# Kernel tuning notes

Measured on AMD Instinct MI355X. Metric: run time of the kernel, lower is better.

The kernel has to match this reference:

```python
import jax, jax.numpy as jnp
import numpy as np

N_HEADS = 16
HEAD_DIM = 64
DIM = 1024
B, L = 2, 2048


def setup_inputs() -> dict:
    key = jax.random.key(0)
    ks = jax.random.split(key, 6)
    s = 1.0 / np.sqrt(DIM)
    return {
        "X": jax.random.normal(ks[0], (B, L, DIM), dtype=jnp.float32),
        "attention_mask": jax.random.randint(ks[1], (B, L, L), 0, 2, dtype=jnp.int32),
        "Wq": jax.random.normal(ks[2], (DIM, DIM), dtype=jnp.float32) * s,
        "Wk": jax.random.normal(ks[3], (DIM, DIM), dtype=jnp.float32) * s,
        "Wv": jax.random.normal(ks[4], (DIM, DIM), dtype=jnp.float32) * s,
        "Wo": jax.random.normal(ks[5], (DIM, DIM), dtype=jnp.float32) * s,
    }


def reference(X, attention_mask, Wq, Wk, Wv, Wo):
    # Linear weights follow torch convention: (out_features, in_features)
    b, l, _ = X.shape
    Q = (X @ Wq.T).reshape(b, l, N_HEADS, HEAD_DIM).transpose(0, 2, 1, 3)  # [B,H,L,D]
    K = (X @ Wk.T).reshape(b, l, N_HEADS, HEAD_DIM).transpose(0, 2, 1, 3)
    V = (X @ Wv.T).reshape(b, l, N_HEADS, HEAD_DIM).transpose(0, 2, 1, 3)
    scores = jnp.einsum("bhqd,bhkd->bhqk", Q, K) / np.sqrt(HEAD_DIM)  # [B,H,L,L]
    mask = (attention_mask[:, None, :, :] == 0)  # broadcast over heads
    scores = jnp.where(mask, jnp.float32(-1e20), scores)
    probs = jax.nn.softmax(scores, axis=-1)
    # dropout is identity in eval/inference mode
    ctx = jnp.einsum("bhqk,bhkd->bhqd", probs, V)  # [B,H,L,D]
    ctx = ctx.transpose(0, 2, 1, 3).reshape(b, l, N_HEADS * HEAD_DIM)
    return ctx @ Wo.T
```

## Files before the change

kernel.cpp:

```cpp
#include <hip/hip_runtime.h>
#include <cstddef>


typedef __bf16 bf16x8 __attribute__((ext_vector_type(8)));
typedef __bf16 bf16x4 __attribute__((ext_vector_type(4)));
typedef float  f32x4  __attribute__((ext_vector_type(4)));
typedef short  s16x4  __attribute__((ext_vector_type(4)));

__device__ __forceinline__ void async16(const __bf16* g, __bf16* l) {
  __builtin_amdgcn_global_load_lds((const __attribute__((address_space(1))) unsigned int*)g,
                                   (__attribute__((address_space(3))) unsigned int*)l, 16, 0, 0);
}

__global__ __launch_bounds__(256) void cvt_all(
    const float* __restrict__ X,  const float* __restrict__ Wq, const float* __restrict__ Wk,
    const float* __restrict__ Wv, const float* __restrict__ Wo,
    __bf16* __restrict__ oX,  __bf16* __restrict__ oWq, __bf16* __restrict__ oWk,
    __bf16* __restrict__ oWv, __bf16* __restrict__ oWo) {
  int i = blockIdx.x * 256 + threadIdx.x;
  const float* s; __bf16* d; int off;
  if (i < 1048576)      { s = X;  d = oX;  off = i; }
  else if (i < 1310720) { s = Wq; d = oWq; off = i - 1048576; }
  else if (i < 1572864) { s = Wk; d = oWk; off = i - 1310720; }
  else if (i < 1835008) { s = Wv; d = oWv; off = i - 1572864; }
  else                  { s = Wo; d = oWo; off = i - 1835008; }
  float4 v = ((const float4*)s)[off];
  bf16x4 o;
  o.x = (__bf16)v.x; o.y = (__bf16)v.y; o.z = (__bf16)v.z; o.w = (__bf16)v.w;
  ((bf16x4*)d)[off] = o;
}

__global__ __launch_bounds__(256) void mask_pack(const int* __restrict__ m,
                                                 unsigned long long* __restrict__ pm) {
  int w = blockIdx.x * 4 + (threadIdx.x >> 6);
  int lane = threadIdx.x & 63;
  unsigned long long bits = __ballot(m[(size_t)w * 64 + lane] != 0);
  int b = w >> 16, q = (w >> 5) & 2047, kt = w & 31;
  if (lane == 0) pm[((size_t)b << 16) + kt * 2048 + q] = bits;
}

template<bool OUT_BF16>
__device__ __forceinline__ void gemm128(const __bf16* __restrict__ A, const __bf16* __restrict__ B,
                                        void* __restrict__ C, int lda, int ldb, int ldc,
                                        int m0, int n0, __bf16* As, __bf16* Bs) {
  const int tid = threadIdx.x;
  const int wave = tid >> 6, lane = tid & 63, quad = lane >> 4, l15 = lane & 15;
  const int wm = (wave & 1) * 64, wn = (wave >> 1) * 64;
  const f32x4 z4 = {0.f, 0.f, 0.f, 0.f};
  f32x4 acc[4][4];
#pragma unroll
  for (int i = 0; i < 4; ++i)
#pragma unroll
    for (int j = 0; j < 4; ++j) acc[i][j] = z4;

  for (int k0 = 0; k0 < 1024; k0 += 32) {
#pragma unroll
    for (int s = 0; s < 2; ++s) {
      int p = (wave * 2 + s) * 64 + lane;
      int r = p >> 2;
      int cc = (p & 3) ^ ((r >> 1) & 3);
      async16(A + (size_t)(m0 + r) * lda + (k0 + cc * 8), As + (wave * 2 + s) * 512);
      async16(B + (size_t)(n0 + r) * ldb + (k0 + cc * 8), Bs + (wave * 2 + s) * 512);
    }
    __syncthreads();
    bf16x8 af[4], bfr[4];
#pragma unroll
    for (int i = 0; i < 4; ++i) {
      int r = wm + i * 16 + l15;
      int cc = quad ^ ((r >> 1) & 3);
      af[i] = *(const bf16x8*)(As + r * 32 + cc * 8);
    }
#pragma unroll
    for (int j = 0; j < 4; ++j) {
      int r = wn + j * 16 + l15;
      int cc = quad ^ ((r >> 1) & 3);
      bfr[j] = *(const bf16x8*)(Bs + r * 32 + cc * 8);
    }
#pragma unroll
    for (int i = 0; i < 4; ++i)
#pragma unroll
      for (int j = 0; j < 4; ++j)
        acc[i][j] = __builtin_amdgcn_mfma_f32_16x16x32_bf16(af[i], bfr[j], acc[i][j], 0, 0, 0);
    __syncthreads();
  }
#pragma unroll
  for (int i = 0; i < 4; ++i)
#pragma unroll
    for (int j = 0; j < 4; ++j)
#pragma unroll
      for (int rr = 0; rr < 4; ++rr) {
        int row = m0 + wm + i * 16 + quad * 4 + rr;
        int col = n0 + wn + j * 16 + l15;
        if (OUT_BF16) ((__bf16*)C)[(size_t)row * ldc + col] = (__bf16)acc[i][j][rr];
        else          ((float*)C)[(size_t)row * ldc + col]  = acc[i][j][rr];
      }
}

__global__ __launch_bounds__(256) void qkv_gemm(const __bf16* __restrict__ X,
                                                const __bf16* __restrict__ Wq,
                                                const __bf16* __restrict__ Wk,
                                                const __bf16* __restrict__ Wv,
                                                __bf16* __restrict__ Q, __bf16* __restrict__ K,
                                                __bf16* __restrict__ Vt) {
  __shared__ __bf16 As[4096], Bs[4096];
  int t = blockIdx.x, z = blockIdx.y;
  if (z < 2) {
    int mt = t & 31, nt = t >> 5;
    gemm128<true>(X, z ? Wk : Wq, z ? K : Q, 1024, 1024, 1024, mt * 128, nt * 128, As, Bs);
  } else {
    int mt = t & 7, nt = t >> 3;
    gemm128<true>(Wv, X, Vt, 1024, 1024, 4096, mt * 128, nt * 128, As, Bs);
  }
}

__global__ __launch_bounds__(256) void out_gemm(const __bf16* __restrict__ Ctx,
                                                const __bf16* __restrict__ Wo,
                                                float* __restrict__ Out) {
  __shared__ __bf16 As[4096], Bs[4096];
  int t = blockIdx.x;
  int mt = t & 31, nt = t >> 5;
  gemm128<false>(Ctx, Wo, Out, 1024, 1024, 1024, mt * 128, nt * 128, As, Bs);
}

__global__ __launch_bounds__(256, 2) void attn_kernel(
    const __bf16* __restrict__ Q, const __bf16* __restrict__ K,
    const __bf16* __restrict__ Vt, const unsigned long long* __restrict__ pm,
    __bf16* __restrict__ Ctx) {
  __shared__ __bf16 Ks[2][4096];
  __shared__ __bf16 Vs[2][4096];
  const int tid = threadIdx.x;
  const int wave = tid >> 6, lane = tid & 63, quad = lane >> 4, l15 = lane & 15;
  const int id = blockIdx.x;
  const int qt = id >> 5, hb = id & 31, h = hb & 15, b = hb >> 4;
  const int q0 = qt * 64;

  const __bf16* Qp = Q + (size_t)(b * 2048 + q0 + wave * 16 + l15) * 1024 + h * 64 + quad * 8;
  bf16x8 aq0 = *(const bf16x8*)Qp;
  bf16x8 aq1 = *(const bf16x8*)(Qp + 32);

  const unsigned long long* Pm = pm + ((size_t)b << 16) + q0 + wave * 16 + l15;
  const int l7 = l15 & 7;

  auto stage = [&](int buf, int kv0) {
#pragma unroll
    for (int s = 0; s < 2; ++s) {
      int p = s * 256 + wave * 64 + lane;
      int r = p >> 3, c = (p & 7) ^ (r & 7);
      async16(K  + (size_t)(b * 2048 + kv0 + r) * 1024 + h * 64 + c * 8,
              &Ks[buf][(s * 256 + wave * 64) * 8]);
      async16(Vt + (size_t)(h * 64 + r) * 4096 + b * 2048 + kv0 + c * 8,
              &Vs[buf][(s * 256 + wave * 64) * 8]);
    }
  };

  stage(0, 0);
  unsigned long long mw = Pm[0];

  const f32x4 z4 = {0.f, 0.f, 0.f, 0.f};
  const short one_bf16 = (short)0x3F80;
  const s16x4 vOnes = {one_bf16, one_bf16, one_bf16, one_bf16};
  f32x4 acc[4];
#pragma unroll
  for (int dt = 0; dt < 4; ++dt) acc[dt] = z4;
  f32x4 acc_l = z4;

  for (int t = 0; t < 32; ++t) {
    __syncthreads();
    if (t < 31) stage((t & 1) ^ 1, (t + 1) * 64);

    const __bf16* Kc = Ks[t & 1];
    const __bf16* Vc = Vs[t & 1];

    f32x4 s4[4];
#pragma unroll
    for (int jt = 0; jt < 4; ++jt) {
      int r = jt * 16 + l15;
      bf16x8 k0 = *(const bf16x8*)(Kc + r * 64 + ((quad ^ (r & 7)) * 8));
      bf16x8 k1 = *(const bf16x8*)(Kc + r * 64 + (((4 + quad) ^ (r & 7)) * 8));
      f32x4 tt = z4;
      tt = __builtin_amdgcn_mfma_f32_16x16x32_bf16(k0, aq0, tt, 0, 0, 0);
      tt = __builtin_amdgcn_mfma_f32_16x16x32_bf16(k1, aq1, tt, 0, 0, 0);
      s4[jt] = tt;
    }

    unsigned long long wq = mw >> (quad * 4);
    if (t < 31) mw = Pm[(size_t)(t + 1) * 2048];
    unsigned lo32 = (unsigned)wq, hi32 = (unsigned)(wq >> 32);

#pragma unroll
    for (int kf = 0; kf < 4; ++kf) {
      unsigned bw = (kf < 2) ? lo32 : hi32;
      s16x4 ptk;
#pragma unroll
      for (int rr = 0; rr < 4; ++rr) {
        float e = fmaf(s4[kf][rr], 0.18033688011112042f, -28.853900817779268f);
        e = (bw & (1u << ((kf & 1) * 16 + rr))) ? e : -1e30f;
        float pv = __builtin_amdgcn_exp2f(e);
        ptk[rr] = __builtin_bit_cast(short, (__bf16)pv);
      }
      acc_l = __builtin_amdgcn_mfma_f32_16x16x16bf16_1k(ptk, vOnes, acc_l, 0, 0, 0);
#pragma unroll
      for (int dt = 0; dt < 4; ++dt) {
        int d = dt * 16 + l15;
        s16x4 vb = *(const s16x4*)(Vc + d * 64 + (((kf * 2 + (quad >> 1)) ^ (d & 7)) * 8)
                                   + (quad & 1) * 4);
        acc[dt] = __builtin_amdgcn_mfma_f32_16x16x16bf16_1k(ptk, vb, acc[dt], 0, 0, 0);
      }
    }
  }

  f32x4 inv;
#pragma unroll
  for (int rr = 0; rr < 4; ++rr) inv[rr] = 1.0f / acc_l[rr];
#pragma unroll
  for (int dt = 0; dt < 4; ++dt)
#pragma unroll
    for (int rr = 0; rr < 4; ++rr)
      Ctx[(size_t)(b * 2048 + q0 + wave * 16 + quad * 4 + rr) * 1024 + h * 64 + dt * 16 + l15] =
          (__bf16)(acc[dt][rr] * inv[rr]);
}

extern "C" void kernel_launch(void* const* d_in, const int* in_sizes, int n_in,
                              void* d_out, int out_size, void* d_ws, size_t ws_size,
                              hipStream_t stream) {
  const float* X  = (const float*)d_in[0];
  const int* mask = (const int*)d_in[1];
  const float* Wq = (const float*)d_in[2];
  const float* Wk = (const float*)d_in[3];
  const float* Wv = (const float*)d_in[4];
  const float* Wo = (const float*)d_in[5];

  __bf16* w   = (__bf16*)d_ws;
  __bf16* Xbf = w;
  __bf16* Wqb = Xbf + 4194304;
  __bf16* Wkb = Wqb + 1048576;
  __bf16* Wvb = Wkb + 1048576;
  __bf16* Wob = Wvb + 1048576;
  __bf16* Qb  = Wob + 1048576;
  __bf16* Kb  = Qb + 4194304;
  __bf16* Vtb = Kb + 4194304;
  __bf16* Ctx = Vtb + 4194304;
  unsigned long long* pmt = (unsigned long long*)Wqb;

  cvt_all<<<8192, 256, 0, stream>>>(X, Wq, Wk, Wv, Wo, Xbf, Wqb, Wkb, Wvb, Wob);
  qkv_gemm<<<dim3(256, 3), 256, 0, stream>>>(Xbf, Wqb, Wkb, Wvb, Qb, Kb, Vtb);
  mask_pack<<<32768, 256, 0, stream>>>(mask, pmt);
  attn_kernel<<<1024, 256, 0, stream>>>(Qb, Kb, Vtb, pmt, Ctx);
  out_gemm<<<256, 256, 0, stream>>>(Ctx, Wob, (float*)d_out);
}
```

Before: 232.4 us.

## Process two query sub-tiles per wave to reuse K/V LDS fragments

The attention kernel now gives each wave 32 query rows instead of 16, so a block covers 128 queries and the grid is halved. K and V fragments are loaded from LDS once per KV tile into registers and reused for both query sub-tiles, which halves LDS reads and halves the global K/V staging traffic per query. In exchange, register pressure goes up (8 K fragments, 16 V fragments, doubled accumulators), which could reduce occupancy under launch_bounds(256,2), and with only 512 blocks there is less parallelism to spread across the GPU's compute units.

```diff
diff --git a/kernel.cpp b/kernel.cpp
--- a/kernel.cpp
+++ b/kernel.cpp
@@ -132,14 +132,18 @@
   const int wave = tid >> 6, lane = tid & 63, quad = lane >> 4, l15 = lane & 15;
   const int id = blockIdx.x;
   const int qt = id >> 5, hb = id & 31, h = hb & 15, b = hb >> 4;
-  const int q0 = qt * 64;
-
-  const __bf16* Qp = Q + (size_t)(b * 2048 + q0 + wave * 16 + l15) * 1024 + h * 64 + quad * 8;
-  bf16x8 aq0 = *(const bf16x8*)Qp;
-  bf16x8 aq1 = *(const bf16x8*)(Qp + 32);
-
-  const unsigned long long* Pm = pm + ((size_t)b << 16) + q0 + wave * 16 + l15;
-  const int l7 = l15 & 7;
+  const int q0 = qt * 128;
+  const int qw = q0 + wave * 32;
+
+  bf16x8 aq[2][2];
+#pragma unroll
+  for (int st = 0; st < 2; ++st) {
+    const __bf16* Qp = Q + (size_t)(b * 2048 + qw + st * 16 + l15) * 1024 + h * 64 + quad * 8;
+    aq[st][0] = *(const bf16x8*)Qp;
+    aq[st][1] = *(const bf16x8*)(Qp + 32);
+  }
+
+  const unsigned long long* Pm = pm + ((size_t)b << 16) + qw + l15;
 
   auto stage = [&](int buf, int kv0) {
 #pragma unroll
@@ -154,15 +158,17 @@
   };
 
   stage(0, 0);
-  unsigned long long mw = Pm[0];
+  unsigned long long mw[2] = {Pm[0], Pm[16]};
 
   const f32x4 z4 = {0.f, 0.f, 0.f, 0.f};
   const short one_bf16 = (short)0x3F80;
   const s16x4 vOnes = {one_bf16, one_bf16, one_bf16, one_bf16};
-  f32x4 acc[4];
-#pragma unroll
-  for (int dt = 0; dt < 4; ++dt) acc[dt] = z4;
-  f32x4 acc_l = z4;
+  f32x4 acc[2][4];
+#pragma unroll
+  for (int st = 0; st < 2; ++st)
+#pragma unroll
+    for (int dt = 0; dt < 4; ++dt) acc[st][dt] = z4;
+  f32x4 acc_l[2] = {z4, z4};
 
   for (int t = 0; t < 32; ++t) {
     __syncthreads();
@@ -171,53 +177,69 @@
     const __bf16* Kc = Ks[t & 1];
     const __bf16* Vc = Vs[t & 1];
 
-    f32x4 s4[4];
+    bf16x8 kA[8];
 #pragma unroll
     for (int jt = 0; jt < 4; ++jt) {
       int r = jt * 16 + l15;
-      bf16x8 k0 = *(const bf16x8*)(Kc + r * 64 + ((quad ^ (r & 7)) * 8));
-      bf16x8 k1 = *(const bf16x8*)(Kc + r * 64 + (((4 + quad) ^ (r & 7)) * 8));
-      f32x4 tt = z4;
-      tt = __builtin_amdgcn_mfma_f32_16x16x32_bf16(k0, aq0, tt, 0, 0, 0);
-      tt = __builtin_amdgcn_mfma_f32_16x16x32_bf16(k1, aq1, tt, 0, 0, 0);
-      s4[jt] = tt;
-    }
-
-    unsigned long long wq = mw >> (quad * 4);
-    if (t < 31) mw = Pm[(size_t)(t + 1) * 2048];
-    unsigned lo32 = (unsigned)wq, hi32 = (unsigned)(wq >> 32);
-
-#pragma unroll
-    for (int kf = 0; kf < 4; ++kf) {
-      unsigned bw = (kf < 2) ? lo32 : hi32;
-      s16x4 ptk;
-#pragma unroll
-      for (int rr = 0; rr < 4; ++rr) {
-        float e = fmaf(s4[kf][rr], 0.18033688011112042f, -28.853900817779268f);
-        e = (bw & (1u << ((kf & 1) * 16 + rr))) ? e : -1e30f;
-        float pv = __builtin_amdgcn_exp2f(e);
-        ptk[rr] = __builtin_bit_cast(short, (__bf16)pv);
+      kA[jt * 2]     = *(const bf16x8*)(Kc + r * 64 + ((quad ^ (r & 7)) * 8));
+      kA[jt * 2 + 1] = *(const bf16x8*)(Kc + r * 64 + (((4 + quad) ^ (r & 7)) * 8));
+    }
+    s16x4 vB[4][4];
+#pragma unroll
+    for (int dt = 0; dt < 4; ++dt) {
+      int d = dt * 16 + l15;
+#pragma unroll
+      for (int kf = 0; kf < 4; ++kf)
+        vB[dt][kf] = *(const s16x4*)(Vc + d * 64 + (((kf * 2 + (quad >> 1)) ^ (d & 7)) * 8)
+                                     + (quad & 1) * 4);
+    }
+
+#pragma unroll
+    for (int st = 0; st < 2; ++st) {
+      f32x4 s4[4];
+#pragma unroll
+      for (int jt = 0; jt < 4; ++jt) {
+        f32x4 tt = z4;
+        tt = __builtin_amdgcn_mfma_f32_16x16x32_bf16(kA[jt * 2],     aq[st][0], tt, 0, 0, 0);
+        tt = __builtin_amdgcn_mfma_f32_16x16x32_bf16(kA[jt * 2 + 1], aq[st][1], tt, 0, 0, 0);
+        s4[jt] = tt;
       }
-      acc_l = __builtin_amdgcn_mfma_f32_16x16x16bf16_1k(ptk, vOnes, acc_l, 0, 0, 0);
-#pragma unroll
-      for (int dt = 0; dt < 4; ++dt) {
-        int d = dt * 16 + l15;
-        s16x4 vb = *(const s16x4*)(Vc + d * 64 + (((kf * 2 + (quad >> 1)) ^ (d & 7)) * 8)
-                                   + (quad & 1) * 4);
-        acc[dt] = __builtin_amdgcn_mfma_f32_16x16x16bf16_1k(ptk, vb, acc[dt], 0, 0, 0);
+
+      unsigned long long wq = mw[st] >> (quad * 4);
+      if (t < 31) mw[st] = Pm[(size_t)(t + 1) * 2048 + st * 16];
+      unsigned lo32 = (unsigned)wq, hi32 = (unsigned)(wq >> 32);
+
+#pragma unroll
+      for (int kf = 0; kf < 4; ++kf) {
+        unsigned bw = (kf < 2) ? lo32 : hi32;
+        s16x4 ptk;
+#pragma unroll
+        for (int rr = 0; rr < 4; ++rr) {
+          float e = fmaf(s4[kf][rr], 0.18033688011112042f, -28.853900817779268f);
+          e = (bw & (1u << ((kf & 1) * 16 + rr))) ? e : -1e30f;
+          float pv = __builtin_amdgcn_exp2f(e);
+          ptk[rr] = __builtin_bit_cast(short, (__bf16)pv);
+        }
+        acc_l[st] = __builtin_amdgcn_mfma_f32_16x16x16bf16_1k(ptk, vOnes, acc_l[st], 0, 0, 0);
+#pragma unroll
+        for (int dt = 0; dt < 4; ++dt)
+          acc[st][dt] = __builtin_amdgcn_mfma_f32_16x16x16bf16_1k(ptk, vB[dt][kf], acc[st][dt], 0, 0, 0);
       }
     }
   }
 
-  f32x4 inv;
-#pragma unroll
-  for (int rr = 0; rr < 4; ++rr) inv[rr] = 1.0f / acc_l[rr];
-#pragma unroll
-  for (int dt = 0; dt < 4; ++dt)
-#pragma unroll
-    for (int rr = 0; rr < 4; ++rr)
-      Ctx[(size_t)(b * 2048 + q0 + wave * 16 + quad * 4 + rr) * 1024 + h * 64 + dt * 16 + l15] =
-          (__bf16)(acc[dt][rr] * inv[rr]);
+#pragma unroll
+  for (int st = 0; st < 2; ++st) {
+    f32x4 inv;
+#pragma unroll
+    for (int rr = 0; rr < 4; ++rr) inv[rr] = 1.0f / acc_l[st][rr];
+#pragma unroll
+    for (int dt = 0; dt < 4; ++dt)
+#pragma unroll
+      for (int rr = 0; rr < 4; ++rr)
+        Ctx[(size_t)(b * 2048 + qw + st * 16 + quad * 4 + rr) * 1024 + h * 64 + dt * 16 + l15] =
+            (__bf16)(acc[st][dt][rr] * inv[rr]);
+  }
 }
 
 extern "C" void kernel_launch(void* const* d_in, const int* in_sizes, int n_in,
@@ -245,6 +267,6 @@
   cvt_all<<<8192, 256, 0, stream>>>(X, Wq, Wk, Wv, Wo, Xbf, Wqb, Wkb, Wvb, Wob);
   qkv_gemm<<<dim3(256, 3), 256, 0, stream>>>(Xbf, Wqb, Wkb, Wvb, Qb, Kb, Vtb);
   mask_pack<<<32768, 256, 0, stream>>>(mask, pmt);
-  attn_kernel<<<1024, 256, 0, stream>>>(Qb, Kb, Vtb, pmt, Ctx);
+  attn_kernel<<<512, 256, 0, stream>>>(Qb, Kb, Vtb, pmt, Ctx);
   out_gemm<<<256, 256, 0, stream>>>(Ctx, Wob, (float*)d_out);
 }
```

Result: no change. 234.6 us (+0.9%).
